# Kernel tuning notes

Measured on AMD Instinct MI355X. Metric: run time of the kernel, lower is better.

The kernel has to match this reference:

```python
import jax, jax.numpy as jnp
import numpy as np
import math

TA = 0.6081734479693927            # tet target angle / pi (109.47 deg)
DELTA_THETA_DEG = 12.0             # tet gaussian width (degrees)


def _plm(l, m, x, s):
    """Associated Legendre P_l^m(x) with Condon-Shortley phase, s = sin(theta)."""
    if l == 2:
        if m == 0: return 0.5 * (3 * x ** 2 - 1)
        if m == 1: return -3.0 * x * s
        return 3.0 * s ** 2
    if l == 4:
        if m == 0: return 0.125 * (35 * x ** 4 - 30 * x ** 2 + 3)
        if m == 1: return -2.5 * (7 * x ** 3 - 3 * x) * s
        if m == 2: return 7.5 * (7 * x ** 2 - 1) * s ** 2
        if m == 3: return -105.0 * x * s ** 3
        return 105.0 * s ** 4
    # l == 6
    if m == 0: return (231 * x ** 6 - 315 * x ** 4 + 105 * x ** 2 - 5) / 16.0
    if m == 1: return -(21.0 / 8.0) * (33 * x ** 5 - 30 * x ** 3 + 5 * x) * s
    if m == 2: return (105.0 / 8.0) * (33 * x ** 4 - 18 * x ** 2 + 1) * s ** 2
    if m == 3: return -(315.0 / 2.0) * (11 * x ** 3 - 3 * x) * s ** 3
    if m == 4: return (945.0 / 2.0) * (11 * x ** 2 - 1) * s ** 4
    if m == 5: return -10395.0 * x * s ** 5
    return 10395.0 * s ** 6


def _ql(l, theta, phi, mask, nb):
    """Steinhardt bond-orientational order parameter q_l, shape (M,)."""
    x = jnp.cos(theta)
    s = jnp.sin(theta)  # theta in [0, pi] so s >= 0
    acc = 0.0
    for m in range(l + 1):
        nlm = math.sqrt((2 * l + 1) / (4 * math.pi)
                        * math.factorial(l - m) / math.factorial(l + m))
        P = nlm * _plm(l, m, x, s)                      # (M, K)
        re = jnp.sum(P * jnp.cos(m * phi) * mask, axis=1) / nb
        im = jnp.sum(P * jnp.sin(m * phi) * mask, axis=1) / nb
        w = 1.0 if m == 0 else 2.0                      # |Y_{l,-m}| = |Y_{l,m}|
        acc = acc + w * (re ** 2 + im ** 2)
    return jnp.sqrt(4 * math.pi / (2 * l + 1) * acc)


def _forward(positions, atom_indices, neighbor_indices, valid_mask):
    mask = valid_mask.astype(positions.dtype)           # (M, K)
    maskb = valid_mask > 0
    safe_idx = jnp.where(maskb, neighbor_indices, 0)
    neigh_pos = positions[safe_idx]                     # (M, K, 3) gather
    center = positions[atom_indices]                    # (M, 3)

    vec = neigh_pos - center[:, None, :]
    dist = jnp.linalg.norm(vec, axis=-1)                # (M, K)
    unit = vec / (dist[..., None] + 1e-10)
    cos_t = jnp.clip(unit[..., 2], -1.0 + 1e-7, 1.0 - 1e-7)
    theta = jnp.arccos(cos_t) * mask
    phi = jnp.arctan2(unit[..., 1], unit[..., 0]) * mask
    unit = unit * mask[..., None]

    cn = jnp.sum(mask, axis=1)                          # coordination number
    nb = jnp.maximum(cn, 1.0)

    # tetrahedral OP: gaussian of pairwise neighbor-neighbor angles
    K = mask.shape[1]
    cos_ang = jnp.clip(jnp.einsum('mkd,mld->mkl', unit, unit),
                       -1.0 + 1e-7, 1.0 - 1e-7)
    ang = jnp.arccos(cos_ang)                           # (M, K, K)
    pair_mask = (mask[:, :, None] * mask[:, None, :]
                 * (1.0 - jnp.eye(K, dtype=mask.dtype)))
    theta_t = TA * math.pi
    sigma = DELTA_THETA_DEG * math.pi / 180.0
    gauss = jnp.exp(-0.5 * ((ang - theta_t) / sigma) ** 2) * pair_mask
    n_pairs = jnp.maximum(cn * (cn - 1.0), 1.0)
    tet = jnp.sum(gauss, axis=(1, 2)) / n_pairs

    q2 = _ql(2, theta, phi, mask, nb)
    q4 = _ql(4, theta, phi, mask, nb)
    q6 = _ql(6, theta, phi, mask, nb)
    return cn, tet, q2, q4, q6


def setup_inputs() -> dict:
    key = jax.random.key(0)
    k0, k1, k2, k3 = jax.random.split(key, 4)
    N, M, K = 80000, 80000, 20
    positions = jax.random.normal(k0, (N, 3), dtype=jnp.float32)
    atom_indices = jax.random.randint(k1, (M,), 0, N, dtype=jnp.int32)
    neighbor_indices = jax.random.randint(k2, (M, K), 0, N, dtype=jnp.int32)
    valid_mask = jax.random.randint(k3, (M, K), 0, 2, dtype=jnp.int32)
    return {"positions": positions, "atom_indices": atom_indices,
            "neighbor_indices": neighbor_indices, "valid_mask": valid_mask}


def reference(positions, atom_indices, neighbor_indices, valid_mask):
    return _forward(positions, atom_indices, neighbor_indices, valid_mask)
```

## Files before the change

### kernel.cpp

```cpp
#include <hip/hip_runtime.h>
#include <math.h>

#define KNBR 20
#define BLK  256
#define GRP  8
#define APB  (BLK / GRP)
#define MAXP 190
#define PERSIST 2048
#define GLUT 1024

#define THETA_T  1.9106332362490186f
#define INV_SIG  4.7746482927568605f
#define PI_F     3.14159265358979323846f

__device__ __forceinline__ float gauss_at(int k) {
    const float d  = fmaf((float)k, 2.0f / GLUT, -1.0f);
    const float dc = fminf(fmaxf(d, -0.9999999f), 0.9999999f);
    const float ad = fabsf(dc);
    const float pq = fmaf(fmaf(fmaf(-0.0187293f, ad, 0.0742610f), ad,
                          -0.2121144f), ad, 1.5707288f) * sqrtf(1.f - ad);
    const float ang = (dc >= 0.f) ? pq : PI_F - pq;
    const float tt = (ang - THETA_T) * INV_SIG;
    return __expf(-0.5f * tt * tt);
}

template<bool EXACT>
__global__ __launch_bounds__(BLK, 8)
void op_kernel(const float* __restrict__ pos,
               const int*   __restrict__ aidx,
               const int*   __restrict__ nidx,
               const int*   __restrict__ vmsk,
               float*       __restrict__ out,
               int M, int NT)
{
    __shared__ float4 su[APB * KNBR];
    __shared__ unsigned short lut[MAXP];
    __shared__ float glut[GLUT + 1];

    const int tid = threadIdx.x;
    if (tid < MAXP) {
        const int j = (int)((1.0f + sqrtf(fmaf(8.f, (float)tid, 1.0f))) * 0.5f);
        lut[tid] = (unsigned short)((tid - ((j * (j - 1)) >> 1)) | (j << 8));
    }
    for (int k = tid; k <= GLUT; k += BLK)
        glut[k] = gauss_at(k);
    __syncthreads();

    const int r   = tid & (GRP - 1);
    const int g   = tid / GRP;
    const int sub = (tid & 63) >> 3;
    float4* row = &su[g * KNBR];

    int t = blockIdx.x;
    if (t >= NT) return;

    int i = t * APB + g;
    int is = EXACT ? i : min(i, M - 1);
    int a  = aidx[is];
    int ri = is * KNBR;
    int n0 = nidx[ri + r];
    int v0 = (EXACT || i < M) ? vmsk[ri + r] : 0;
    int n1 = nidx[ri + 8 + r];
    int v1 = (EXACT || i < M) ? vmsk[ri + 8 + r] : 0;
    int n2 = 0, v2 = 0;
    if (r < 4) { n2 = nidx[ri + 16 + r]; v2 = (EXACT || i < M) ? vmsk[ri + 16 + r] : 0; }

    while (true) {
        const int tn = t + gridDim.x;
        int aN = 0, n0N = 0, v0N = 0, n1N = 0, v1N = 0, n2N = 0, v2N = 0, iN = 0;
        if (tn < NT) {
            iN = tn * APB + g;
            const int isN = EXACT ? iN : min(iN, M - 1);
            aN = aidx[isN];
            const int rN = isN * KNBR;
            n0N = nidx[rN + r];
            v0N = (EXACT || iN < M) ? vmsk[rN + r] : 0;
            n1N = nidx[rN + 8 + r];
            v1N = (EXACT || iN < M) ? vmsk[rN + 8 + r] : 0;
            if (r < 4) { n2N = nidx[rN + 16 + r]; v2N = (EXACT || iN < M) ? vmsk[rN + 16 + r] : 0; }
        }

        const int use2 = (r < 4) & (v2 != 0);
        const int s0i = (v0 != 0) ? n0 : 0;
        const int s1i = (v1 != 0) ? n1 : 0;
        const int s2i = use2 ? n2 : 0;
        const float cx  = pos[3*a],   cy  = pos[3*a+1],   cz  = pos[3*a+2];
        const float p0x = pos[3*s0i], p0y = pos[3*s0i+1], p0z = pos[3*s0i+2];
        const float p1x = pos[3*s1i], p1y = pos[3*s1i+1], p1z = pos[3*s1i+2];
        const float p2x = pos[3*s2i], p2y = pos[3*s2i+1], p2z = pos[3*s2i+2];

        const unsigned long long bal0 = __ballot(v0 != 0);
        const unsigned long long bal1 = __ballot(v1 != 0);
        const unsigned long long bal2 = __ballot(use2 != 0);
        const unsigned int b0 = (unsigned int)(bal0 >> (sub * 8)) & 0xFFu;
        const unsigned int b1 = (unsigned int)(bal1 >> (sub * 8)) & 0xFFu;
        const unsigned int b2 = (unsigned int)(bal2 >> (sub * 8)) & 0xFu;
        const unsigned int mask20 = b0 | (b1 << 8) | (b2 << 16);
        const int total = __popc(mask20);

        if (v0 != 0) {
            const float vx = p0x - cx, vy = p0y - cy, vz = p0z - cz;
            const float d2 = fmaf(vx, vx, fmaf(vy, vy, vz * vz));
            const int   zed = d2 < 1e-24f;
            const float inv = __builtin_amdgcn_rcpf(sqrtf(d2) + 1e-10f);
            const int slot = __popc(mask20 & ((1u << r) - 1u));
            row[slot] = make_float4(zed ? 1.f : vx * inv,
                                    zed ? 0.f : vy * inv,
                                    zed ? 0.f : vz * inv,
                                    zed ? 0.f : 1.f);
        }
        if (v1 != 0) {
            const float vx = p1x - cx, vy = p1y - cy, vz = p1z - cz;
            const float d2 = fmaf(vx, vx, fmaf(vy, vy, vz * vz));
            const int   zed = d2 < 1e-24f;
            const float inv = __builtin_amdgcn_rcpf(sqrtf(d2) + 1e-10f);
            const int slot = __popc(mask20 & ((1u << (8 + r)) - 1u));
            row[slot] = make_float4(zed ? 1.f : vx * inv,
                                    zed ? 0.f : vy * inv,
                                    zed ? 0.f : vz * inv,
                                    zed ? 0.f : 1.f);
        }
        if (use2) {
            const float vx = p2x - cx, vy = p2y - cy, vz = p2z - cz;
            const float d2 = fmaf(vx, vx, fmaf(vy, vy, vz * vz));
            const int   zed = d2 < 1e-24f;
            const float inv = __builtin_amdgcn_rcpf(sqrtf(d2) + 1e-10f);
            const int slot = __popc(mask20 & ((1u << (16 + r)) - 1u));
            row[slot] = make_float4(zed ? 1.f : vx * inv,
                                    zed ? 0.f : vy * inv,
                                    zed ? 0.f : vz * inv,
                                    zed ? 0.f : 1.f);
        }

        const int npairs = (total * (total - 1)) >> 1;
        float m1 = 0.f, m2 = 0.f, m3 = 0.f, gsum = 0.f;
        for (int p = r; p < npairs; p += GRP) {
            const unsigned short w = lut[p];
            const float4 A = row[w & 0xFF];
            const float4 B = row[w >> 8];
            const float dsh = fmaf(A.x, B.x, fmaf(A.y, B.y, A.z * B.z));
            const float dtt = dsh * A.w * B.w;

            const float e  = dsh * dsh;
            const float e2 = e * e;
            m1 += e;
            m2 += e2;
            m3 = fmaf(e2, e, m3);

            float fx = fmaf(dtt, (float)(GLUT / 2), (float)(GLUT / 2) + 0.5f);
            fx = fminf(fmaxf(fx, 0.f), (float)GLUT + 0.49f);
            gsum += glut[(int)fx];
        }

#define RED(v) { v += __shfl_xor(v,1); v += __shfl_xor(v,2); v += __shfl_xor(v,4); }
        RED(m1) RED(m2) RED(m3) RED(gsum)
#undef RED

        const float fnp = (float)npairs;
        const float s2 = fmaf(1.5f, m1, -0.5f * fnp);
        const float s4 = fmaf(4.375f, m2, fmaf(-3.75f, m1, 0.375f * fnp));
        const float s6 = fmaf(14.4375f, m3,
                         fmaf(-19.6875f, m2, fmaf(6.5625f, m1, -0.3125f * fnp)));

        const float cn = (float)total;
        const float invnb = __builtin_amdgcn_rcpf(fmaxf(cn, 1.f));
        const float tet = gsum * __builtin_amdgcn_rcpf(fmaxf(fnp, 0.5f));
        const float q2v = invnb * sqrtf(fmaxf(fmaf(2.f, s2, cn), 0.f));
        const float q4v = invnb * sqrtf(fmaxf(fmaf(2.f, s4, cn), 0.f));
        const float q6v = invnb * sqrtf(fmaxf(fmaf(2.f, s6, cn), 0.f));

        float val = cn;
        val = (r == 1) ? tet : val;
        val = (r == 2) ? q2v : val;
        val = (r == 3) ? q4v : val;
        val = (r == 4) ? q6v : val;
        if (r < 5 && (EXACT || i < M))
            out[r * M + i] = val;

        if (tn >= NT) break;
        t = tn; i = iN; a = aN;
        n0 = n0N; v0 = v0N; n1 = n1N; v1 = v1N; n2 = n2N; v2 = v2N;
    }
}

extern "C" void kernel_launch(void* const* d_in, const int* in_sizes, int n_in,
                              void* d_out, int out_size, void* d_ws, size_t ws_size,
                              hipStream_t stream) {
    const float* pos  = (const float*)d_in[0];
    const int*   aidx = (const int*)d_in[1];
    const int*   nidx = (const int*)d_in[2];
    const int*   vmsk = (const int*)d_in[3];
    float* out = (float*)d_out;
    const int M = in_sizes[1];
    const int NT = (M + APB - 1) / APB;
    const int grid = NT < PERSIST ? NT : PERSIST;
    if (M % APB == 0)
        op_kernel<true><<<grid, BLK, 0, stream>>>(pos, aidx, nidx, vmsk, out, M, NT);
    else
        op_kernel<false><<<grid, BLK, 0, stream>>>(pos, aidx, nidx, vmsk, out, M, NT);
}
```

Baseline: 16.72 us.

## Replace persistent grid-stride loop with one-tile-per-block launch and pad LDS rows

Drops the persistent kernel, which looped over tiles with software prefetch of the next tile's indices, and launches one block per 32-atom tile (2500 blocks). Each block now builds its Gaussian LUT and pair LUT once and handles a single tile, so that table setup is repeated per block rather than amortised across tiles. The per-group shared row stride goes from 20 to 21 float4 to reduce LDS bank conflicts. The change trades the cross-tile prefetch overlap for simpler control flow, but the extra per-block init of the 1025-entry exp table becomes noticeable overhead.

```diff
diff --git a/kernel.cpp b/kernel.cpp
--- a/kernel.cpp
+++ b/kernel.cpp
@@ -5,8 +5,8 @@
 #define BLK  256
 #define GRP  8
 #define APB  (BLK / GRP)
+#define RST  21
 #define MAXP 190
-#define PERSIST 2048
 #define GLUT 1024
 
 #define THETA_T  1.9106332362490186f
@@ -31,9 +31,9 @@
                const int*   __restrict__ nidx,
                const int*   __restrict__ vmsk,
                float*       __restrict__ out,
-               int M, int NT)
+               int M)
 {
-    __shared__ float4 su[APB * KNBR];
+    __shared__ float4 su[APB * RST];
     __shared__ unsigned short lut[MAXP];
     __shared__ float glut[GLUT + 1];
 
@@ -49,138 +49,117 @@
     const int r   = tid & (GRP - 1);
     const int g   = tid / GRP;
     const int sub = (tid & 63) >> 3;
-    float4* row = &su[g * KNBR];
+    float4* row = &su[g * RST];
 
-    int t = blockIdx.x;
-    if (t >= NT) return;
+    const int i  = blockIdx.x * APB + g;
+    const int is = EXACT ? i : min(i, M - 1);
+    const int ok = EXACT || (i < M);
 
-    int i = t * APB + g;
-    int is = EXACT ? i : min(i, M - 1);
-    int a  = aidx[is];
-    int ri = is * KNBR;
-    int n0 = nidx[ri + r];
-    int v0 = (EXACT || i < M) ? vmsk[ri + r] : 0;
-    int n1 = nidx[ri + 8 + r];
-    int v1 = (EXACT || i < M) ? vmsk[ri + 8 + r] : 0;
+    const int a  = aidx[is];
+    const int ri = is * KNBR;
+    const int n0 = nidx[ri + r];
+    const int v0 = ok ? vmsk[ri + r] : 0;
+    const int n1 = nidx[ri + 8 + r];
+    const int v1 = ok ? vmsk[ri + 8 + r] : 0;
     int n2 = 0, v2 = 0;
-    if (r < 4) { n2 = nidx[ri + 16 + r]; v2 = (EXACT || i < M) ? vmsk[ri + 16 + r] : 0; }
+    if (r < 4) { n2 = nidx[ri + 16 + r]; v2 = ok ? vmsk[ri + 16 + r] : 0; }
 
-    while (true) {
-        const int tn = t + gridDim.x;
-        int aN = 0, n0N = 0, v0N = 0, n1N = 0, v1N = 0, n2N = 0, v2N = 0, iN = 0;
-        if (tn < NT) {
-            iN = tn * APB + g;
-            const int isN = EXACT ? iN : min(iN, M - 1);
-            aN = aidx[isN];
-            const int rN = isN * KNBR;
-            n0N = nidx[rN + r];
-            v0N = (EXACT || iN < M) ? vmsk[rN + r] : 0;
-            n1N = nidx[rN + 8 + r];
-            v1N = (EXACT || iN < M) ? vmsk[rN + 8 + r] : 0;
-            if (r < 4) { n2N = nidx[rN + 16 + r]; v2N = (EXACT || iN < M) ? vmsk[rN + 16 + r] : 0; }
-        }
+    const int use2 = (r < 4) & (v2 != 0);
+    const int s0i = (v0 != 0) ? n0 : 0;
+    const int s1i = (v1 != 0) ? n1 : 0;
+    const int s2i = use2 ? n2 : 0;
+    const float cx  = pos[3*a],   cy  = pos[3*a+1],   cz  = pos[3*a+2];
+    const float p0x = pos[3*s0i], p0y = pos[3*s0i+1], p0z = pos[3*s0i+2];
+    const float p1x = pos[3*s1i], p1y = pos[3*s1i+1], p1z = pos[3*s1i+2];
+    const float p2x = pos[3*s2i], p2y = pos[3*s2i+1], p2z = pos[3*s2i+2];
 
-        const int use2 = (r < 4) & (v2 != 0);
-        const int s0i = (v0 != 0) ? n0 : 0;
-        const int s1i = (v1 != 0) ? n1 : 0;
-        const int s2i = use2 ? n2 : 0;
-        const float cx  = pos[3*a],   cy  = pos[3*a+1],   cz  = pos[3*a+2];
-        const float p0x = pos[3*s0i], p0y = pos[3*s0i+1], p0z = pos[3*s0i+2];
-        const float p1x = pos[3*s1i], p1y = pos[3*s1i+1], p1z = pos[3*s1i+2];
-        const float p2x = pos[3*s2i], p2y = pos[3*s2i+1], p2z = pos[3*s2i+2];
+    const unsigned long long bal0 = __ballot(v0 != 0);
+    const unsigned long long bal1 = __ballot(v1 != 0);
+    const unsigned long long bal2 = __ballot(use2 != 0);
+    const unsigned int b0 = (unsigned int)(bal0 >> (sub * 8)) & 0xFFu;
+    const unsigned int b1 = (unsigned int)(bal1 >> (sub * 8)) & 0xFFu;
+    const unsigned int b2 = (unsigned int)(bal2 >> (sub * 8)) & 0xFu;
+    const unsigned int mask20 = b0 | (b1 << 8) | (b2 << 16);
+    const int total = __popc(mask20);
 
-        const unsigned long long bal0 = __ballot(v0 != 0);
-        const unsigned long long bal1 = __ballot(v1 != 0);
-        const unsigned long long bal2 = __ballot(use2 != 0);
-        const unsigned int b0 = (unsigned int)(bal0 >> (sub * 8)) & 0xFFu;
-        const unsigned int b1 = (unsigned int)(bal1 >> (sub * 8)) & 0xFFu;
-        const unsigned int b2 = (unsigned int)(bal2 >> (sub * 8)) & 0xFu;
-        const unsigned int mask20 = b0 | (b1 << 8) | (b2 << 16);
-        const int total = __popc(mask20);
+    if (v0 != 0) {
+        const float vx = p0x - cx, vy = p0y - cy, vz = p0z - cz;
+        const float d2 = fmaf(vx, vx, fmaf(vy, vy, vz * vz));
+        const int   zed = d2 < 1e-24f;
+        const float inv = __builtin_amdgcn_rcpf(sqrtf(d2) + 1e-10f);
+        const int slot = __popc(mask20 & ((1u << r) - 1u));
+        row[slot] = make_float4(zed ? 1.f : vx * inv,
+                                zed ? 0.f : vy * inv,
+                                zed ? 0.f : vz * inv,
+                                zed ? 0.f : 1.f);
+    }
+    if (v1 != 0) {
+        const float vx = p1x - cx, vy = p1y - cy, vz = p1z - cz;
+        const float d2 = fmaf(vx, vx, fmaf(vy, vy, vz * vz));
+        const int   zed = d2 < 1e-24f;
+        const float inv = __builtin_amdgcn_rcpf(sqrtf(d2) + 1e-10f);
+        const int slot = __popc(mask20 & ((1u << (8 + r)) - 1u));
+        row[slot] = make_float4(zed ? 1.f : vx * inv,
+                                zed ? 0.f : vy * inv,
+                                zed ? 0.f : vz * inv,
+                                zed ? 0.f : 1.f);
+    }
+    if (use2) {
+        const float vx = p2x - cx, vy = p2y - cy, vz = p2z - cz;
+        const float d2 = fmaf(vx, vx, fmaf(vy, vy, vz * vz));
+        const int   zed = d2 < 1e-24f;
+        const float inv = __builtin_amdgcn_rcpf(sqrtf(d2) + 1e-10f);
+        const int slot = __popc(mask20 & ((1u << (16 + r)) - 1u));
+        row[slot] = make_float4(zed ? 1.f : vx * inv,
+                                zed ? 0.f : vy * inv,
+                                zed ? 0.f : vz * inv,
+                                zed ? 0.f : 1.f);
+    }
 
-        if (v0 != 0) {
-            const float vx = p0x - cx, vy = p0y - cy, vz = p0z - cz;
-            const float d2 = fmaf(vx, vx, fmaf(vy, vy, vz * vz));
-            const int   zed = d2 < 1e-24f;
-            const float inv = __builtin_amdgcn_rcpf(sqrtf(d2) + 1e-10f);
-            const int slot = __popc(mask20 & ((1u << r) - 1u));
-            row[slot] = make_float4(zed ? 1.f : vx * inv,
-                                    zed ? 0.f : vy * inv,
-                                    zed ? 0.f : vz * inv,
-                                    zed ? 0.f : 1.f);
-        }
-        if (v1 != 0) {
-            const float vx = p1x - cx, vy = p1y - cy, vz = p1z - cz;
-            const float d2 = fmaf(vx, vx, fmaf(vy, vy, vz * vz));
-            const int   zed = d2 < 1e-24f;
-            const float inv = __builtin_amdgcn_rcpf(sqrtf(d2) + 1e-10f);
-            const int slot = __popc(mask20 & ((1u << (8 + r)) - 1u));
-            row[slot] = make_float4(zed ? 1.f : vx * inv,
-                                    zed ? 0.f : vy * inv,
-                                    zed ? 0.f : vz * inv,
-                                    zed ? 0.f : 1.f);
-        }
-        if (use2) {
-            const float vx = p2x - cx, vy = p2y - cy, vz = p2z - cz;
-            const float d2 = fmaf(vx, vx, fmaf(vy, vy, vz * vz));
-            const int   zed = d2 < 1e-24f;
-            const float inv = __builtin_amdgcn_rcpf(sqrtf(d2) + 1e-10f);
-            const int slot = __popc(mask20 & ((1u << (16 + r)) - 1u));
-            row[slot] = make_float4(zed ? 1.f : vx * inv,
-                                    zed ? 0.f : vy * inv,
-                                    zed ? 0.f : vz * inv,
-                                    zed ? 0.f : 1.f);
-        }
+    const int npairs = (total * (total - 1)) >> 1;
+    float m1 = 0.f, m2 = 0.f, m3 = 0.f, gsum = 0.f;
+    for (int p = r; p < npairs; p += GRP) {
+        const unsigned short w = lut[p];
+        const float4 A = row[w & 0xFF];
+        const float4 B = row[w >> 8];
+        const float dsh = fmaf(A.x, B.x, fmaf(A.y, B.y, A.z * B.z));
+        const float dtt = dsh * A.w * B.w;
 
-        const int npairs = (total * (total - 1)) >> 1;
-        float m1 = 0.f, m2 = 0.f, m3 = 0.f, gsum = 0.f;
-        for (int p = r; p < npairs; p += GRP) {
-            const unsigned short w = lut[p];
-            const float4 A = row[w & 0xFF];
-            const float4 B = row[w >> 8];
-            const float dsh = fmaf(A.x, B.x, fmaf(A.y, B.y, A.z * B.z));
-            const float dtt = dsh * A.w * B.w;
+        const float e  = dsh * dsh;
+        const float e2 = e * e;
+        m1 += e;
+        m2 += e2;
+        m3 = fmaf(e2, e, m3);
 
-            const float e  = dsh * dsh;
-            const float e2 = e * e;
-            m1 += e;
-            m2 += e2;
-            m3 = fmaf(e2, e, m3);
-
-            float fx = fmaf(dtt, (float)(GLUT / 2), (float)(GLUT / 2) + 0.5f);
-            fx = fminf(fmaxf(fx, 0.f), (float)GLUT + 0.49f);
-            gsum += glut[(int)fx];
-        }
+        float fx = fmaf(dtt, (float)(GLUT / 2), (float)(GLUT / 2) + 0.5f);
+        fx = fminf(fmaxf(fx, 0.f), (float)GLUT + 0.49f);
+        gsum += glut[(int)fx];
+    }
 
 #define RED(v) { v += __shfl_xor(v,1); v += __shfl_xor(v,2); v += __shfl_xor(v,4); }
-        RED(m1) RED(m2) RED(m3) RED(gsum)
+    RED(m1) RED(m2) RED(m3) RED(gsum)
 #undef RED
 
-        const float fnp = (float)npairs;
-        const float s2 = fmaf(1.5f, m1, -0.5f * fnp);
-        const float s4 = fmaf(4.375f, m2, fmaf(-3.75f, m1, 0.375f * fnp));
-        const float s6 = fmaf(14.4375f, m3,
-                         fmaf(-19.6875f, m2, fmaf(6.5625f, m1, -0.3125f * fnp)));
+    const float fnp = (float)npairs;
+    const float s2 = fmaf(1.5f, m1, -0.5f * fnp);
+    const float s4 = fmaf(4.375f, m2, fmaf(-3.75f, m1, 0.375f * fnp));
+    const float s6 = fmaf(14.4375f, m3,
+                     fmaf(-19.6875f, m2, fmaf(6.5625f, m1, -0.3125f * fnp)));
 
-        const float cn = (float)total;
-        const float invnb = __builtin_amdgcn_rcpf(fmaxf(cn, 1.f));
-        const float tet = gsum * __builtin_amdgcn_rcpf(fmaxf(fnp, 0.5f));
-        const float q2v = invnb * sqrtf(fmaxf(fmaf(2.f, s2, cn), 0.f));
-        const float q4v = invnb * sqrtf(fmaxf(fmaf(2.f, s4, cn), 0.f));
-        const float q6v = invnb * sqrtf(fmaxf(fmaf(2.f, s6, cn), 0.f));
+    const float cn = (float)total;
+    const float invnb = __builtin_amdgcn_rcpf(fmaxf(cn, 1.f));
+    const float tet = gsum * __builtin_amdgcn_rcpf(fmaxf(fnp, 0.5f));
+    const float q2v = invnb * sqrtf(fmaxf(fmaf(2.f, s2, cn), 0.f));
+    const float q4v = invnb * sqrtf(fmaxf(fmaf(2.f, s4, cn), 0.f));
+    const float q6v = invnb * sqrtf(fmaxf(fmaf(2.f, s6, cn), 0.f));
 
-        float val = cn;
-        val = (r == 1) ? tet : val;
-        val = (r == 2) ? q2v : val;
-        val = (r == 3) ? q4v : val;
-        val = (r == 4) ? q6v : val;
-        if (r < 5 && (EXACT || i < M))
-            out[r * M + i] = val;
-
-        if (tn >= NT) break;
-        t = tn; i = iN; a = aN;
-        n0 = n0N; v0 = v0N; n1 = n1N; v1 = v1N; n2 = n2N; v2 = v2N;
-    }
+    float val = cn;
+    val = (r == 1) ? tet : val;
+    val = (r == 2) ? q2v : val;
+    val = (r == 3) ? q4v : val;
+    val = (r == 4) ? q6v : val;
+    if (r < 5 && ok)
+        out[r * M + i] = val;
 }
 
 extern "C" void kernel_launch(void* const* d_in, const int* in_sizes, int n_in,
@@ -193,9 +172,8 @@
     float* out = (float*)d_out;
     const int M = in_sizes[1];
     const int NT = (M + APB - 1) / APB;
-    const int grid = NT < PERSIST ? NT : PERSIST;
     if (M % APB == 0)
-        op_kernel<true><<<grid, BLK, 0, stream>>>(pos, aidx, nidx, vmsk, out, M, NT);
+        op_kernel<true><<<NT, BLK, 0, stream>>>(pos, aidx, nidx, vmsk, out, M);
     else
-        op_kernel<false><<<grid, BLK, 0, stream>>>(pos, aidx, nidx, vmsk, out, M, NT);
+        op_kernel<false><<<NT, BLK, 0, stream>>>(pos, aidx, nidx, vmsk, out, M);
 }
```

New measurement: 17.26 us. +3.2%, slower.
